# Kernel tuning notes

Hardware: AMD Instinct MI355X
Metric: run time of the kernel (lower is better)

Reference implementation:

```python
import jax, jax.numpy as jnp
import numpy as np

B, Q, K, D = 16, 2048, 2048, 512


def setup_inputs() -> dict:
    key = jax.random.key(0)
    kq, kk, kv, kl = jax.random.split(key, 4)
    queries = jax.random.normal(kq, (B, Q, D), dtype=jnp.float32)
    keys = jax.random.normal(kk, (B, K, D), dtype=jnp.float32)
    values = jax.random.normal(kv, (B, K, D), dtype=jnp.float32)
    # lengths in [1, K] so no row is fully masked
    valid_lens = jax.random.randint(kl, (B,), 1, K + 1, dtype=jnp.int32)
    return {"queries": queries, "keys": keys, "values": values, "valid_lens": valid_lens}


def reference(queries, keys, values, valid_lens):
    # scores: [B, Q, K]
    scale = 1.0 / jnp.sqrt(jnp.asarray(queries.shape[-1], queries.dtype))
    scores = jnp.einsum('bqd,bkd->bqk', queries, keys) * scale
    # 1D valid_lens: per-batch key-length mask (positions >= len are masked)
    key_pos = jnp.arange(scores.shape[-1])  # [K]
    mask = key_pos[None, None, :] >= valid_lens[:, None, None]  # [B, 1->Q, K]
    scores = jnp.where(mask, -jnp.inf, scores)
    weights = jax.nn.softmax(scores, axis=-1)  # [B, Q, K]
    # dropout is identity in eval mode (deterministic reference)
    context = jnp.einsum('bqk,bkd->bqd', weights, values)  # [B, Q, D]
    return context, weights
```

## Files before the change

kernel.cpp:

```cpp
#include <hip/hip_runtime.h>
#include <stdint.h>

typedef __bf16 bf16_t;
typedef bf16_t bf16x8 __attribute__((ext_vector_type(8)));
typedef bf16_t bf16x4_t __attribute__((ext_vector_type(4)));
typedef float f32x4 __attribute__((ext_vector_type(4)));

#define NB 16
#define NQ 2048
#define NK 2048
#define ND 512
#define SCALE 0.04419417382415922f

typedef __attribute__((address_space(3))) uint32_t lds_u32;
typedef __attribute__((address_space(1))) const uint32_t glb_u32;

__device__ __forceinline__ float4 ld4(const float* p) { return *(const float4*)p; }

__device__ __forceinline__ f32x4 mfma16(bf16x8 a, bf16x8 b, f32x4 c) {
  return __builtin_amdgcn_mfma_f32_16x16x32_bf16(a, b, c, 0, 0, 0);
}

__global__ __launch_bounds__(256) void prep_kernel(const float* __restrict__ Qf,
                                                   const float* __restrict__ Kf,
                                                   const float* __restrict__ Vf,
                                                   bf16_t* __restrict__ Qb,
                                                   bf16_t* __restrict__ Kb,
                                                   bf16_t* __restrict__ VT,
                                                   const int* __restrict__ lens) {
  int x = blockIdx.x;
  int b = blockIdx.y;
  int z = blockIdx.z;
  int t = threadIdx.x;

  if (z == 2) {
    int kb = x >> 2, dq = (x & 3) * 128;
    if (kb * 32 >= lens[b]) return;
    const float* vsrc = Vf + ((size_t)b * NK + kb * 32) * ND;
    bf16_t* dst = VT + ((size_t)(b * 64 + kb)) * (512 * 32);
    __shared__ alignas(16) bf16_t Ls[32][128];
#pragma unroll
    for (int i = 0; i < 4; ++i) {
      int p = i * 256 + t;
      int k = p >> 5, c4 = p & 31;
      float4 v = ld4(vsrc + (size_t)k * ND + dq + c4 * 4);
      union { bf16_t h[4]; uint2 u; } pk;
      pk.h[0] = (bf16_t)v.x; pk.h[1] = (bf16_t)v.y;
      pk.h[2] = (bf16_t)v.z; pk.h[3] = (bf16_t)v.w;
      *(uint2*)(&Ls[k][c4 * 4]) = pk.u;
    }
    __syncthreads();
    int d = dq + (t >> 1);
    int h = t & 1;
    int sr = d >> 1;
#pragma unroll
    for (int gg = 0; gg < 2; ++gg) {
      int g = h * 2 + gg;
      bf16x8 v;
#pragma unroll
      for (int j = 0; j < 8; ++j) v[j] = Ls[g * 8 + j][d - dq];
      int slot = (((d & 1) << 2) | g) ^ (sr & 7);
      *(bf16x8*)(dst + ((size_t)sr * 8 + slot) * 8) = v;
    }
    return;
  }

  const float* src = z ? Kf : Qf;
  bf16_t* dst = z ? Kb : Qb;
  int rt = x >> 4, kt = x & 15;
  const float* s = src + ((size_t)b * 2048 + (size_t)rt * 128) * 512 + kt * 32;
  bf16_t* dtile = dst + (((size_t)b * 16 + rt) * 16 + kt) * 4096;
#pragma unroll
  for (int i = 0; i < 2; ++i) {
    int d = i * 256 + t;
    int r = d >> 2, slot = d & 3;
    int c = slot ^ ((r >> 1) & 3);
    const float* p = s + (size_t)r * 512 + c * 8;
    float4 v0 = ld4(p), v1 = ld4(p + 4);
    bf16x8 o;
    o[0] = (bf16_t)v0.x; o[1] = (bf16_t)v0.y; o[2] = (bf16_t)v0.z; o[3] = (bf16_t)v0.w;
    o[4] = (bf16_t)v1.x; o[5] = (bf16_t)v1.y; o[6] = (bf16_t)v1.z; o[7] = (bf16_t)v1.w;
    *(bf16x8*)(dtile + (size_t)d * 8) = o;
  }
}

__global__ __launch_bounds__(512, 4) void qk_kernel(const bf16_t* __restrict__ Qb,
                                                    const bf16_t* __restrict__ Kb,
                                                    float* __restrict__ P,
                                                    float* __restrict__ psum,
                                                    const int* __restrict__ lens) {
  int bid = blockIdx.x;
  int swz = (bid & 7) * 256 + (bid >> 3);
  int b = swz >> 7;
  int qt = (swz >> 4) & 7;
  int nt = swz & 15;

  int len = lens[b];
  int q0 = qt * 256;
  int col0 = nt * 128;
  if (col0 >= len) return;

  __shared__ alignas(16) bf16_t As[2][8192];
  __shared__ alignas(16) bf16_t Bs[2][4096];
  __shared__ float rsm[256];

  int t = threadIdx.x;
  int lane = t & 63;
  int wid = t >> 6;
  int wm = wid >> 1, wn = wid & 1;
  int l15 = lane & 15, l4 = lane >> 4;

  float* prow = P + ((size_t)b * NQ + q0) * NK;
  const bf16_t* qbase = Qb + ((size_t)b * 256) * 4096;
  const bf16_t* ktile = Kb + (((size_t)b * 16 + nt) * 16) * 4096;

  f32x4 acc[4][4];
  f32x4 zz = {0.f, 0.f, 0.f, 0.f};
#pragma unroll
  for (int mi = 0; mi < 4; ++mi)
#pragma unroll
    for (int ni = 0; ni < 4; ++ni) acc[mi][ni] = zz;

  auto stage = [&](int kt2, int buf) {
#pragma unroll
    for (int u = 0; u < 2; ++u) {
      const bf16_t* qa = qbase + ((size_t)((qt * 2 + u) * 16 + kt2)) * 4096 + t * 8;
      __builtin_amdgcn_global_load_lds((glb_u32*)qa,
                                       (lds_u32*)(&As[buf][u * 4096 + wid * 512]), 16, 0, 0);
    }
    const bf16_t* ka = ktile + (size_t)kt2 * 4096 + t * 8;
    __builtin_amdgcn_global_load_lds((glb_u32*)ka,
                                     (lds_u32*)(&Bs[buf][wid * 512]), 16, 0, 0);
  };

  auto compute = [&](int buf) {
    bf16x8 af[4], bv[4];
#pragma unroll
    for (int mi = 0; mi < 4; ++mi) {
      int row = wm * 64 + mi * 16 + l15;
      int u = row >> 7, r7 = row & 127;
      int ch = r7 * 4 + (l4 ^ ((r7 >> 1) & 3));
      af[mi] = *(const bf16x8*)(&As[buf][u * 4096 + ch * 8]);
    }
#pragma unroll
    for (int ni = 0; ni < 4; ++ni) {
      int row = wn * 64 + ni * 16 + l15;
      int ch = row * 4 + (l4 ^ ((row >> 1) & 3));
      bv[ni] = *(const bf16x8*)(&Bs[buf][ch * 8]);
    }
#pragma unroll
    for (int mi = 0; mi < 4; ++mi)
#pragma unroll
      for (int ni = 0; ni < 4; ++ni)
        acc[mi][ni] = mfma16(af[mi], bv[ni], acc[mi][ni]);
  };

  stage(0, 0);
  __syncthreads();
#pragma unroll 1
  for (int kt2 = 0; kt2 < 16; ++kt2) {
    if (kt2 + 1 < 16) stage(kt2 + 1, (kt2 + 1) & 1);
    compute(kt2 & 1);
    __syncthreads();
  }

  float rsum[4][4];
#pragma unroll
  for (int mi = 0; mi < 4; ++mi)
#pragma unroll
    for (int r = 0; r < 4; ++r) rsum[mi][r] = 0.f;

#pragma unroll
  for (int mi = 0; mi < 4; ++mi) {
#pragma unroll
    for (int ni = 0; ni < 4; ++ni) {
      int col = col0 + wn * 64 + ni * 16 + l15;
      bool valid = col < len;
#pragma unroll
      for (int r = 0; r < 4; ++r) {
        float e = valid ? __expf(acc[mi][ni][r] * SCALE) : 0.f;
        bf16_t eb = (bf16_t)e;
        rsum[mi][r] += (float)eb;
        bf16_t* purow =
            (bf16_t*)(prow + (size_t)(wm * 64 + mi * 16 + l4 * 4 + r) * NK) + 2048;
        purow[col] = eb;
      }
    }
  }

#pragma unroll
  for (int off = 1; off < 16; off <<= 1)
#pragma unroll
    for (int mi = 0; mi < 4; ++mi)
#pragma unroll
      for (int r = 0; r < 4; ++r)
        rsum[mi][r] += __shfl_xor(rsum[mi][r], off, 64);

  if (wn == 0 && l15 == 0) {
#pragma unroll
    for (int mi = 0; mi < 4; ++mi)
#pragma unroll
      for (int r = 0; r < 4; ++r)
        rsm[wm * 64 + mi * 16 + l4 * 4 + r] = rsum[mi][r];
  }
  __syncthreads();
  if (wn == 1 && l15 == 0) {
#pragma unroll
    for (int mi = 0; mi < 4; ++mi)
#pragma unroll
      for (int r = 0; r < 4; ++r) {
        int row = wm * 64 + mi * 16 + l4 * 4 + r;
        psum[((size_t)b * 16 + nt) * NQ + q0 + row] = rsum[mi][r] + rsm[row];
      }
  }
}

__global__ __launch_bounds__(512, 4) void pv_kernel(float* __restrict__ P,
                                                    const bf16_t* __restrict__ VT,
                                                    float* __restrict__ ctx,
                                                    const float* __restrict__ psum,
                                                    const int* __restrict__ lens) {
  int bid = blockIdx.x;
  int b = bid & 15, qt = bid >> 4;
  int q0 = qt * 64;
  int len = lens[b];
  int nsteps = (len + 31) >> 5;
  int nvalid = (len + 127) >> 7;

  __shared__ alignas(16) bf16_t Ps[2][64 * 32];
  __shared__ float rcp[64];

  int t = threadIdx.x;
  if (t < 64) {
    float s = 0.f;
    for (int i = 0; i < nvalid; ++i) s += psum[((size_t)b * 16 + i) * NQ + q0 + t];
    rcp[t] = 1.0f / s;
  }
  __syncthreads();

  float* prow = P + ((size_t)b * NQ + q0) * NK;
  const bf16_t* vtb = VT + ((size_t)b * 64) * (512 * 32);

  int lane = t & 63, wid = t >> 6;
  int l15 = lane & 15, l4 = lane >> 4;

  f32x4 acc[4][4];
  f32x4 zz = {0.f, 0.f, 0.f, 0.f};
#pragma unroll
  for (int mi = 0; mi < 4; ++mi)
#pragma unroll
    for (int ni = 0; ni < 4; ++ni) acc[mi][ni] = zz;

  int srow = t >> 3, sc4 = t & 7;
  float rr = rcp[srow];
  const bf16_t* purow = (const bf16_t*)(prow + (size_t)srow * NK) + 2048;

  int vchunk[4];
#pragma unroll
  for (int ni = 0; ni < 4; ++ni) {
    int d = wid * 64 + ni * 16 + l15;
    vchunk[ni] = ((d >> 1) * 8 + ((((d & 1) << 2) | l4) ^ ((d >> 1) & 7))) * 8;
  }

  bf16x4_t pld;

  auto stage_load = [&](int ks) {
    pld = *(const bf16x4_t*)(purow + ks * 32 + sc4 * 4);
  };
  auto stage_finish = [&](int ks, int buf) {
    float4 w;
    w.x = (float)pld[0] * rr; w.y = (float)pld[1] * rr;
    w.z = (float)pld[2] * rr; w.w = (float)pld[3] * rr;
    *(float4*)(prow + (size_t)srow * NK + ks * 32 + sc4 * 4) = w;
    int sr = srow >> 1;
    int slot = (((srow & 1) << 2) | (sc4 >> 1)) ^ (sr & 7);
    union { bf16_t h[4]; uint2 u; } pk;
    pk.h[0] = (bf16_t)w.x; pk.h[1] = (bf16_t)w.y;
    pk.h[2] = (bf16_t)w.z; pk.h[3] = (bf16_t)w.w;
    *(uint2*)(&Ps[buf][((size_t)sr * 8 + slot) * 8 + (sc4 & 1) * 4]) = pk.u;
  };
  auto compute = [&](int ks, int cur) {
    const bf16_t* vsrc = vtb + (size_t)ks * (512 * 32);
    bf16x8 bv[4];
#pragma unroll
    for (int ni = 0; ni < 4; ++ni)
      bv[ni] = *(const bf16x8*)(vsrc + vchunk[ni]);
    bf16x8 af[4];
#pragma unroll
    for (int mi = 0; mi < 4; ++mi) {
      int row = mi * 16 + l15;
      af[mi] = *(const bf16x8*)(&Ps[cur][((row >> 1) * 8 + ((((row & 1) << 2) | l4) ^ ((row >> 1) & 7))) * 8]);
    }
#pragma unroll
    for (int mi = 0; mi < 4; ++mi)
#pragma unroll
      for (int ni = 0; ni < 4; ++ni)
        acc[mi][ni] = mfma16(af[mi], bv[ni], acc[mi][ni]);
  };

  stage_load(0);
  stage_finish(0, 0);
  __syncthreads();
#pragma unroll 1
  for (int ks = 0; ks < nsteps; ++ks) {
    int cur = ks & 1;
    if (ks + 1 < nsteps) stage_load(ks + 1);
    compute(ks, cur);
    if (ks + 1 < nsteps) stage_finish(ks + 1, cur ^ 1);
    __syncthreads();
  }

  {
    float4 z = make_float4(0.f, 0.f, 0.f, 0.f);
    for (int c = nsteps * 32 + sc4 * 4; c < NK; c += 32)
      *(float4*)(prow + (size_t)srow * NK + c) = z;
  }

  float* crow = ctx + ((size_t)b * NQ + q0) * ND + wid * 64;
#pragma unroll
  for (int mi = 0; mi < 4; ++mi)
#pragma unroll
    for (int ni = 0; ni < 4; ++ni)
#pragma unroll
      for (int r = 0; r < 4; ++r)
        crow[(size_t)(mi * 16 + l4 * 4 + r) * ND + ni * 16 + l15] = acc[mi][ni][r];
}

extern "C" void kernel_launch(void* const* d_in, const int* in_sizes, int n_in,
                              void* d_out, int out_size, void* d_ws, size_t ws_size,
                              hipStream_t stream) {
  const float* Q = (const float*)d_in[0];
  const float* K = (const float*)d_in[1];
  const float* V = (const float*)d_in[2];
  const int* lens = (const int*)d_in[3];

  float* ctx = (float*)d_out;
  float* P = ctx + (size_t)NB * NQ * ND;

  float* psum = (float*)d_ws;
  char* base = (char*)d_ws + (size_t)NB * 16 * NQ * sizeof(float);
  bf16_t* Qb = (bf16_t*)base;
  bf16_t* Kb = (bf16_t*)(base + (size_t)NB * NQ * ND * 2);
  bf16_t* VT = (bf16_t*)(base + (size_t)2 * NB * NQ * ND * 2);

  prep_kernel<<<dim3(256, 16, 3), 256, 0, stream>>>(Q, K, V, Qb, Kb, VT, lens);
  qk_kernel<<<dim3(2048), 512, 0, stream>>>(Qb, Kb, P, psum, lens);
  pv_kernel<<<dim3(512), 512, 0, stream>>>(P, VT, ctx, psum, lens);
}
```

Baseline: 271.1 us.

## Keep Q block resident in LDS and sweep all key tiles per QK block

The QK kernel now converts its 128-row fp32 Q block to bf16 directly into LDS once, then loops over all valid 256-column key tiles. It writes exp values per tile and accumulates row sums across tiles, so psum becomes one value per row instead of per-tile partials. This removes the Q conversion pass from the prep kernel and the repeated Q loads from global memory. In exchange, only 256 large blocks run at one block per CU (128KB LDS), and blocks whose batch has a long valid length do more work, which risks poor occupancy and load imbalance.

```diff
diff --git a/kernel.cpp b/kernel.cpp
--- a/kernel.cpp
+++ b/kernel.cpp
@@ -21,10 +21,8 @@
   return __builtin_amdgcn_mfma_f32_16x16x32_bf16(a, b, c, 0, 0, 0);
 }
 
-__global__ __launch_bounds__(256) void prep_kernel(const float* __restrict__ Qf,
-                                                   const float* __restrict__ Kf,
+__global__ __launch_bounds__(256) void prep_kernel(const float* __restrict__ Kf,
                                                    const float* __restrict__ Vf,
-                                                   bf16_t* __restrict__ Qb,
                                                    bf16_t* __restrict__ Kb,
                                                    bf16_t* __restrict__ VT,
                                                    const int* __restrict__ lens) {
@@ -33,7 +31,7 @@
   int z = blockIdx.z;
   int t = threadIdx.x;
 
-  if (z == 2) {
+  if (z == 1) {
     int kb = x >> 2, dq = (x & 3) * 128;
     if (kb * 32 >= lens[b]) return;
     const float* vsrc = Vf + ((size_t)b * NK + kb * 32) * ND;
@@ -65,11 +63,9 @@
     return;
   }
 
-  const float* src = z ? Kf : Qf;
-  bf16_t* dst = z ? Kb : Qb;
   int rt = x >> 4, kt = x & 15;
-  const float* s = src + ((size_t)b * 2048 + (size_t)rt * 128) * 512 + kt * 32;
-  bf16_t* dtile = dst + (((size_t)b * 16 + rt) * 16 + kt) * 4096;
+  const float* s = Kf + ((size_t)b * 2048 + (size_t)rt * 128) * 512 + kt * 32;
+  bf16_t* dtile = Kb + (((size_t)b * 16 + rt) * 16 + kt) * 4096;
 #pragma unroll
   for (int i = 0; i < 2; ++i) {
     int d = i * 256 + t;
@@ -84,35 +80,45 @@
   }
 }
 
-__global__ __launch_bounds__(512, 4) void qk_kernel(const bf16_t* __restrict__ Qb,
+__global__ __launch_bounds__(512, 1) void qk_kernel(const float* __restrict__ Qf,
                                                     const bf16_t* __restrict__ Kb,
                                                     float* __restrict__ P,
                                                     float* __restrict__ psum,
                                                     const int* __restrict__ lens) {
   int bid = blockIdx.x;
-  int swz = (bid & 7) * 256 + (bid >> 3);
-  int b = swz >> 7;
-  int qt = (swz >> 4) & 7;
-  int nt = swz & 15;
-
+  int b = bid & 15, qt = bid >> 4;
   int len = lens[b];
-  int q0 = qt * 256;
-  int col0 = nt * 128;
-  if (col0 >= len) return;
-
-  __shared__ alignas(16) bf16_t As[2][8192];
-  __shared__ alignas(16) bf16_t Bs[2][4096];
-  __shared__ float rsm[256];
+  int q0 = qt * 128;
+  int nvp = (len + 255) >> 8;
+  int nsteps = nvp * 16;
+
+  __shared__ alignas(16) bf16_t As[128 * 512];
+  __shared__ alignas(16) bf16_t Bs[2][256 * 32];
 
   int t = threadIdx.x;
   int lane = t & 63;
   int wid = t >> 6;
-  int wm = wid >> 1, wn = wid & 1;
+  int wm = wid >> 2, wn = wid & 3;
   int l15 = lane & 15, l4 = lane >> 4;
 
   float* prow = P + ((size_t)b * NQ + q0) * NK;
-  const bf16_t* qbase = Qb + ((size_t)b * 256) * 4096;
-  const bf16_t* ktile = Kb + (((size_t)b * 16 + nt) * 16) * 4096;
+  const bf16_t* kbase = Kb + ((size_t)b * 256) * 4096;
+
+  {
+    const float* qsrc = Qf + ((size_t)b * NQ + q0) * ND;
+#pragma unroll
+    for (int i = 0; i < 16; ++i) {
+      int g = i * 512 + t;
+      int row = g >> 6, ch = g & 63;
+      const float* p = qsrc + (size_t)row * ND + ch * 8;
+      float4 v0 = ld4(p), v1 = ld4(p + 4);
+      bf16x8 o;
+      o[0] = (bf16_t)v0.x; o[1] = (bf16_t)v0.y; o[2] = (bf16_t)v0.z; o[3] = (bf16_t)v0.w;
+      o[4] = (bf16_t)v1.x; o[5] = (bf16_t)v1.y; o[6] = (bf16_t)v1.z; o[7] = (bf16_t)v1.w;
+      int slot = (ch & 56) | ((ch & 7) ^ (row & 7));
+      *(bf16x8*)(&As[row * 512 + slot * 8]) = o;
+    }
+  }
 
   f32x4 acc[4][4];
   f32x4 zz = {0.f, 0.f, 0.f, 0.f};
@@ -121,32 +127,37 @@
 #pragma unroll
     for (int ni = 0; ni < 4; ++ni) acc[mi][ni] = zz;
 
-  auto stage = [&](int kt2, int buf) {
+  float rsum[4][4];
+#pragma unroll
+  for (int mi = 0; mi < 4; ++mi)
+#pragma unroll
+    for (int r = 0; r < 4; ++r) rsum[mi][r] = 0.f;
+
+  auto stage = [&](int s, int buf) {
+    int ntp = s >> 4, kt = s & 15;
 #pragma unroll
     for (int u = 0; u < 2; ++u) {
-      const bf16_t* qa = qbase + ((size_t)((qt * 2 + u) * 16 + kt2)) * 4096 + t * 8;
-      __builtin_amdgcn_global_load_lds((glb_u32*)qa,
-                                       (lds_u32*)(&As[buf][u * 4096 + wid * 512]), 16, 0, 0);
-    }
-    const bf16_t* ka = ktile + (size_t)kt2 * 4096 + t * 8;
-    __builtin_amdgcn_global_load_lds((glb_u32*)ka,
-                                     (lds_u32*)(&Bs[buf][wid * 512]), 16, 0, 0);
-  };
-
-  auto compute = [&](int buf) {
+      const bf16_t* ka = kbase + ((size_t)((ntp * 2 + u) * 16 + kt)) * 4096 + t * 8;
+      __builtin_amdgcn_global_load_lds((glb_u32*)ka,
+                                       (lds_u32*)(&Bs[buf][u * 4096 + wid * 512]), 16, 0, 0);
+    }
+  };
+
+  auto compute = [&](int kt, int buf) {
     bf16x8 af[4], bv[4];
 #pragma unroll
     for (int mi = 0; mi < 4; ++mi) {
       int row = wm * 64 + mi * 16 + l15;
-      int u = row >> 7, r7 = row & 127;
+      int ch = kt * 4 + l4;
+      int slot = (ch & 56) | ((ch & 7) ^ (row & 7));
+      af[mi] = *(const bf16x8*)(&As[row * 512 + slot * 8]);
+    }
+#pragma unroll
+    for (int ni = 0; ni < 4; ++ni) {
+      int c = wn * 64 + ni * 16 + l15;
+      int u = c >> 7, r7 = c & 127;
       int ch = r7 * 4 + (l4 ^ ((r7 >> 1) & 3));
-      af[mi] = *(const bf16x8*)(&As[buf][u * 4096 + ch * 8]);
-    }
-#pragma unroll
-    for (int ni = 0; ni < 4; ++ni) {
-      int row = wn * 64 + ni * 16 + l15;
-      int ch = row * 4 + (l4 ^ ((row >> 1) & 3));
-      bv[ni] = *(const bf16x8*)(&Bs[buf][ch * 8]);
+      bv[ni] = *(const bf16x8*)(&Bs[buf][u * 4096 + ch * 8]);
     }
 #pragma unroll
     for (int mi = 0; mi < 4; ++mi)
@@ -157,35 +168,33 @@
 
   stage(0, 0);
   __syncthreads();
+
 #pragma unroll 1
-  for (int kt2 = 0; kt2 < 16; ++kt2) {
-    if (kt2 + 1 < 16) stage(kt2 + 1, (kt2 + 1) & 1);
-    compute(kt2 & 1);
+  for (int s = 0; s < nsteps; ++s) {
+    if (s + 1 < nsteps) stage(s + 1, (s + 1) & 1);
+    compute(s & 15, s & 1);
+    if ((s & 15) == 15) {
+      int col0 = (s >> 4) * 256;
+#pragma unroll
+      for (int mi = 0; mi < 4; ++mi) {
+#pragma unroll
+        for (int ni = 0; ni < 4; ++ni) {
+          int col = col0 + wn * 64 + ni * 16 + l15;
+          bool valid = col < len;
+#pragma unroll
+          for (int r = 0; r < 4; ++r) {
+            float e = valid ? __expf(acc[mi][ni][r] * SCALE) : 0.f;
+            bf16_t eb = (bf16_t)e;
+            rsum[mi][r] += (float)eb;
+            bf16_t* purow =
+                (bf16_t*)(prow + (size_t)(wm * 64 + mi * 16 + l4 * 4 + r) * NK) + 2048;
+            purow[col] = eb;
+          }
+          acc[mi][ni] = zz;
+        }
+      }
+    }
     __syncthreads();
-  }
-
-  float rsum[4][4];
-#pragma unroll
-  for (int mi = 0; mi < 4; ++mi)
-#pragma unroll
-    for (int r = 0; r < 4; ++r) rsum[mi][r] = 0.f;
-
-#pragma unroll
-  for (int mi = 0; mi < 4; ++mi) {
-#pragma unroll
-    for (int ni = 0; ni < 4; ++ni) {
-      int col = col0 + wn * 64 + ni * 16 + l15;
-      bool valid = col < len;
-#pragma unroll
-      for (int r = 0; r < 4; ++r) {
-        float e = valid ? __expf(acc[mi][ni][r] * SCALE) : 0.f;
-        bf16_t eb = (bf16_t)e;
-        rsum[mi][r] += (float)eb;
-        bf16_t* purow =
-            (bf16_t*)(prow + (size_t)(wm * 64 + mi * 16 + l4 * 4 + r) * NK) + 2048;
-        purow[col] = eb;
-      }
-    }
   }
 
 #pragma unroll
@@ -196,23 +205,17 @@
       for (int r = 0; r < 4; ++r)
         rsum[mi][r] += __shfl_xor(rsum[mi][r], off, 64);
 
-  if (wn == 0 && l15 == 0) {
+  float* rsm = (float*)&Bs[0][0];
+  if (l15 == 0) {
 #pragma unroll
     for (int mi = 0; mi < 4; ++mi)
 #pragma unroll
       for (int r = 0; r < 4; ++r)
-        rsm[wm * 64 + mi * 16 + l4 * 4 + r] = rsum[mi][r];
+        rsm[wn * 128 + wm * 64 + mi * 16 + l4 * 4 + r] = rsum[mi][r];
   }
   __syncthreads();
-  if (wn == 1 && l15 == 0) {
-#pragma unroll
-    for (int mi = 0; mi < 4; ++mi)
-#pragma unroll
-      for (int r = 0; r < 4; ++r) {
-        int row = wm * 64 + mi * 16 + l4 * 4 + r;
-        psum[((size_t)b * 16 + nt) * NQ + q0 + row] = rsum[mi][r] + rsm[row];
-      }
-  }
+  if (t < 128)
+    psum[(size_t)b * NQ + q0 + t] = rsm[t] + rsm[128 + t] + rsm[256 + t] + rsm[384 + t];
 }
 
 __global__ __launch_bounds__(512, 4) void pv_kernel(float* __restrict__ P,
@@ -225,17 +228,12 @@
   int q0 = qt * 64;
   int len = lens[b];
   int nsteps = (len + 31) >> 5;
-  int nvalid = (len + 127) >> 7;
 
   __shared__ alignas(16) bf16_t Ps[2][64 * 32];
   __shared__ float rcp[64];
 
   int t = threadIdx.x;
-  if (t < 64) {
-    float s = 0.f;
-    for (int i = 0; i < nvalid; ++i) s += psum[((size_t)b * 16 + i) * NQ + q0 + t];
-    rcp[t] = 1.0f / s;
-  }
+  if (t < 64) rcp[t] = 1.0f / psum[(size_t)b * NQ + q0 + t];
   __syncthreads();
 
   float* prow = P + ((size_t)b * NQ + q0) * NK;
@@ -338,12 +336,11 @@
   float* P = ctx + (size_t)NB * NQ * ND;
 
   float* psum = (float*)d_ws;
-  char* base = (char*)d_ws + (size_t)NB * 16 * NQ * sizeof(float);
-  bf16_t* Qb = (bf16_t*)base;
-  bf16_t* Kb = (bf16_t*)(base + (size_t)NB * NQ * ND * 2);
-  bf16_t* VT = (bf16_t*)(base + (size_t)2 * NB * NQ * ND * 2);
-
-  prep_kernel<<<dim3(256, 16, 3), 256, 0, stream>>>(Q, K, V, Qb, Kb, VT, lens);
-  qk_kernel<<<dim3(2048), 512, 0, stream>>>(Qb, Kb, P, psum, lens);
+  char* base = (char*)d_ws + (size_t)NB * NQ * sizeof(float);
+  bf16_t* Kb = (bf16_t*)base;
+  bf16_t* VT = (bf16_t*)(base + (size_t)NB * NQ * ND * 2);
+
+  prep_kernel<<<dim3(256, 16, 2), 256, 0, stream>>>(K, V, Kb, VT, lens);
+  qk_kernel<<<dim3(256), 512, 0, stream>>>(Q, Kb, P, psum, lens);
   pv_kernel<<<dim3(512), 512, 0, stream>>>(P, VT, ctx, psum, lens);
 }
```

Result: slower. 306.5 us (+13.1%).

## Make PV kernel persistent with atomic work queue and 32-row query tiles

Applied to the files above, without the earlier changes.

The PV kernel becomes persistent: 512 blocks repeatedly take work items from a global atomic counter, and each item covers a 32-query tile rather than a 64-query tile, giving 1024 items. The aim is to balance the uneven per-batch work caused by variable valid lengths, since long-length batches no longer pin whole blocks while others sit idle. In exchange only half the threads stage P in each item, each V fragment is reused across fewer rows, and every launch adds a memset plus an atomic and extra barriers per item.

```diff
diff --git a/kernel.cpp b/kernel.cpp
--- a/kernel.cpp
+++ b/kernel.cpp
@@ -11,6 +11,7 @@
 #define NK 2048
 #define ND 512
 #define SCALE 0.04419417382415922f
+#define NITEMS 1024
 
 typedef __attribute__((address_space(3))) uint32_t lds_u32;
 typedef __attribute__((address_space(1))) const uint32_t glb_u32;
@@ -219,41 +220,16 @@
                                                     const bf16_t* __restrict__ VT,
                                                     float* __restrict__ ctx,
                                                     const float* __restrict__ psum,
-                                                    const int* __restrict__ lens) {
-  int bid = blockIdx.x;
-  int b = bid & 15, qt = bid >> 4;
-  int q0 = qt * 64;
-  int len = lens[b];
-  int nsteps = (len + 31) >> 5;
-  int nvalid = (len + 127) >> 7;
-
-  __shared__ alignas(16) bf16_t Ps[2][64 * 32];
-  __shared__ float rcp[64];
+                                                    const int* __restrict__ lens,
+                                                    int* __restrict__ counter) {
+  __shared__ alignas(16) bf16_t Ps[2][32 * 32];
+  __shared__ float rcp[32];
+  __shared__ int itm;
 
   int t = threadIdx.x;
-  if (t < 64) {
-    float s = 0.f;
-    for (int i = 0; i < nvalid; ++i) s += psum[((size_t)b * 16 + i) * NQ + q0 + t];
-    rcp[t] = 1.0f / s;
-  }
-  __syncthreads();
-
-  float* prow = P + ((size_t)b * NQ + q0) * NK;
-  const bf16_t* vtb = VT + ((size_t)b * 64) * (512 * 32);
-
   int lane = t & 63, wid = t >> 6;
   int l15 = lane & 15, l4 = lane >> 4;
-
-  f32x4 acc[4][4];
-  f32x4 zz = {0.f, 0.f, 0.f, 0.f};
-#pragma unroll
-  for (int mi = 0; mi < 4; ++mi)
-#pragma unroll
-    for (int ni = 0; ni < 4; ++ni) acc[mi][ni] = zz;
-
   int srow = t >> 3, sc4 = t & 7;
-  float rr = rcp[srow];
-  const bf16_t* purow = (const bf16_t*)(prow + (size_t)srow * NK) + 2048;
 
   int vchunk[4];
 #pragma unroll
@@ -262,68 +238,105 @@
     vchunk[ni] = ((d >> 1) * 8 + ((((d & 1) << 2) | l4) ^ ((d >> 1) & 7))) * 8;
   }
 
-  bf16x4_t pld;
-
-  auto stage_load = [&](int ks) {
-    pld = *(const bf16x4_t*)(purow + ks * 32 + sc4 * 4);
-  };
-  auto stage_finish = [&](int ks, int buf) {
-    float4 w;
-    w.x = (float)pld[0] * rr; w.y = (float)pld[1] * rr;
-    w.z = (float)pld[2] * rr; w.w = (float)pld[3] * rr;
-    *(float4*)(prow + (size_t)srow * NK + ks * 32 + sc4 * 4) = w;
-    int sr = srow >> 1;
-    int slot = (((srow & 1) << 2) | (sc4 >> 1)) ^ (sr & 7);
-    union { bf16_t h[4]; uint2 u; } pk;
-    pk.h[0] = (bf16_t)w.x; pk.h[1] = (bf16_t)w.y;
-    pk.h[2] = (bf16_t)w.z; pk.h[3] = (bf16_t)w.w;
-    *(uint2*)(&Ps[buf][((size_t)sr * 8 + slot) * 8 + (sc4 & 1) * 4]) = pk.u;
-  };
-  auto compute = [&](int ks, int cur) {
-    const bf16_t* vsrc = vtb + (size_t)ks * (512 * 32);
-    bf16x8 bv[4];
-#pragma unroll
-    for (int ni = 0; ni < 4; ++ni)
-      bv[ni] = *(const bf16x8*)(vsrc + vchunk[ni]);
-    bf16x8 af[4];
-#pragma unroll
-    for (int mi = 0; mi < 4; ++mi) {
-      int row = mi * 16 + l15;
-      af[mi] = *(const bf16x8*)(&Ps[cur][((row >> 1) * 8 + ((((row & 1) << 2) | l4) ^ ((row >> 1) & 7))) * 8]);
-    }
-#pragma unroll
-    for (int mi = 0; mi < 4; ++mi)
+  for (;;) {
+    if (t == 0) itm = atomicAdd(counter, 1);
+    __syncthreads();
+    int item = itm;
+    if (item >= NITEMS) break;
+    int b = item >> 6;
+    int qt = item & 63;
+    int q0 = qt * 32;
+    int len = lens[b];
+    int nsteps = (len + 31) >> 5;
+    int nvalid = (len + 127) >> 7;
+
+    if (t < 32) {
+      float s = 0.f;
+      for (int i = 0; i < nvalid; ++i) s += psum[((size_t)b * 16 + i) * NQ + q0 + t];
+      rcp[t] = 1.0f / s;
+    }
+    __syncthreads();
+
+    float* prow = P + ((size_t)b * NQ + q0) * NK;
+    const bf16_t* vtb = VT + ((size_t)b * 64) * (512 * 32);
+    float rr = (t < 256) ? rcp[srow] : 0.f;
+    const bf16_t* purow = (const bf16_t*)(prow + (size_t)srow * NK) + 2048;
+
+    f32x4 acc[2][4];
+    f32x4 zz = {0.f, 0.f, 0.f, 0.f};
+#pragma unroll
+    for (int mi = 0; mi < 2; ++mi)
+#pragma unroll
+      for (int ni = 0; ni < 4; ++ni) acc[mi][ni] = zz;
+
+    bf16x4_t pld;
+    auto stage_load = [&](int ks) {
+      if (t < 256) pld = *(const bf16x4_t*)(purow + ks * 32 + sc4 * 4);
+    };
+    auto stage_finish = [&](int ks, int buf) {
+      if (t < 256) {
+        float4 w;
+        w.x = (float)pld[0] * rr; w.y = (float)pld[1] * rr;
+        w.z = (float)pld[2] * rr; w.w = (float)pld[3] * rr;
+        *(float4*)(prow + (size_t)srow * NK + ks * 32 + sc4 * 4) = w;
+        int sr = srow >> 1;
+        int slot = (((srow & 1) << 2) | (sc4 >> 1)) ^ (sr & 7);
+        union { bf16_t h[4]; uint2 u; } pk;
+        pk.h[0] = (bf16_t)w.x; pk.h[1] = (bf16_t)w.y;
+        pk.h[2] = (bf16_t)w.z; pk.h[3] = (bf16_t)w.w;
+        *(uint2*)(&Ps[buf][((size_t)sr * 8 + slot) * 8 + (sc4 & 1) * 4]) = pk.u;
+      }
+    };
+    auto compute = [&](int ks, int cur) {
+      const bf16_t* vsrc = vtb + (size_t)ks * (512 * 32);
+      bf16x8 bv[4];
 #pragma unroll
       for (int ni = 0; ni < 4; ++ni)
-        acc[mi][ni] = mfma16(af[mi], bv[ni], acc[mi][ni]);
-  };
-
-  stage_load(0);
-  stage_finish(0, 0);
-  __syncthreads();
+        bv[ni] = *(const bf16x8*)(vsrc + vchunk[ni]);
+      bf16x8 af[2];
+#pragma unroll
+      for (int mi = 0; mi < 2; ++mi) {
+        int row = mi * 16 + l15;
+        af[mi] = *(const bf16x8*)(&Ps[cur][((row >> 1) * 8 + ((((row & 1) << 2) | l4) ^ ((row >> 1) & 7))) * 8]);
+      }
+#pragma unroll
+      for (int mi = 0; mi < 2; ++mi)
+#pragma unroll
+        for (int ni = 0; ni < 4; ++ni)
+          acc[mi][ni] = mfma16(af[mi], bv[ni], acc[mi][ni]);
+    };
+
+    stage_load(0);
+    stage_finish(0, 0);
+    __syncthreads();
 #pragma unroll 1
-  for (int ks = 0; ks < nsteps; ++ks) {
-    int cur = ks & 1;
-    if (ks + 1 < nsteps) stage_load(ks + 1);
-    compute(ks, cur);
-    if (ks + 1 < nsteps) stage_finish(ks + 1, cur ^ 1);
-    __syncthreads();
-  }
-
-  {
-    float4 z = make_float4(0.f, 0.f, 0.f, 0.f);
-    for (int c = nsteps * 32 + sc4 * 4; c < NK; c += 32)
-      *(float4*)(prow + (size_t)srow * NK + c) = z;
-  }
-
-  float* crow = ctx + ((size_t)b * NQ + q0) * ND + wid * 64;
-#pragma unroll
-  for (int mi = 0; mi < 4; ++mi)
-#pragma unroll
-    for (int ni = 0; ni < 4; ++ni)
-#pragma unroll
-      for (int r = 0; r < 4; ++r)
-        crow[(size_t)(mi * 16 + l4 * 4 + r) * ND + ni * 16 + l15] = acc[mi][ni][r];
+    for (int ks = 0; ks < nsteps; ++ks) {
+      int cur = ks & 1;
+      if (ks + 1 < nsteps) stage_load(ks + 1);
+      compute(ks, cur);
+      if (ks == 62 && nsteps == 64) __syncthreads();
+      if (ks + 1 < nsteps) stage_finish(ks + 1, cur ^ 1);
+      __syncthreads();
+    }
+
+    {
+      float4 z = make_float4(0.f, 0.f, 0.f, 0.f);
+      int zr = t >> 4, zc = t & 15;
+      for (int c = nsteps * 32 + zc * 4; c < NK; c += 64)
+        *(float4*)(prow + (size_t)zr * NK + c) = z;
+    }
+
+    float* crow = ctx + ((size_t)b * NQ + q0) * ND + wid * 64;
+#pragma unroll
+    for (int mi = 0; mi < 2; ++mi)
+#pragma unroll
+      for (int ni = 0; ni < 4; ++ni)
+#pragma unroll
+        for (int r = 0; r < 4; ++r)
+          crow[(size_t)(mi * 16 + l4 * 4 + r) * ND + ni * 16 + l15] = acc[mi][ni][r];
+
+    __syncthreads();
+  }
 }
 
 extern "C" void kernel_launch(void* const* d_in, const int* in_sizes, int n_in,
@@ -342,8 +355,10 @@
   bf16_t* Qb = (bf16_t*)base;
   bf16_t* Kb = (bf16_t*)(base + (size_t)NB * NQ * ND * 2);
   bf16_t* VT = (bf16_t*)(base + (size_t)2 * NB * NQ * ND * 2);
+  int* counter = (int*)(base + (size_t)3 * NB * NQ * ND * 2);
 
   prep_kernel<<<dim3(256, 16, 3), 256, 0, stream>>>(Q, K, V, Qb, Kb, VT, lens);
   qk_kernel<<<dim3(2048), 512, 0, stream>>>(Qb, Kb, P, psum, lens);
-  pv_kernel<<<dim3(512), 512, 0, stream>>>(P, VT, ctx, psum, lens);
-}
+  hipMemsetAsync(counter, 0, sizeof(int), stream);
+  pv_kernel<<<dim3(512), 512, 0, stream>>>(P, VT, ctx, psum, lens, counter);
+}
```

New measurement: 309.2 us. 14.0% more time.

## Split weight normalization out of PV kernel and defer context scaling

Applied to the files above, without the earlier changes.

The PV kernel now only stages the unnormalized bf16 probabilities (stored in the upper half of each P row) into LDS and runs the MFMA, then scales the context output by the per-row reciprocal sum at the end. A new wnorm kernel afterwards reads the bf16 data, normalizes it, writes the fp32 weights and zeroes masked columns across the full row. The aim is to take the global fp32 weight stores out of the MFMA loop and use a simple streaming kernel for them. This adds a kernel launch and a second read of the bf16 data, and relies on running wnorm after ctx because both use the same buffer.

```diff
diff --git a/kernel.cpp b/kernel.cpp
--- a/kernel.cpp
+++ b/kernel.cpp
@@ -215,11 +215,11 @@
   }
 }
 
-__global__ __launch_bounds__(512, 4) void pv_kernel(float* __restrict__ P,
-                                                    const bf16_t* __restrict__ VT,
-                                                    float* __restrict__ ctx,
-                                                    const float* __restrict__ psum,
-                                                    const int* __restrict__ lens) {
+__global__ __launch_bounds__(512, 4) void ctx_kernel(const float* __restrict__ P,
+                                                     const bf16_t* __restrict__ VT,
+                                                     float* __restrict__ ctx,
+                                                     const float* __restrict__ psum,
+                                                     const int* __restrict__ lens) {
   int bid = blockIdx.x;
   int b = bid & 15, qt = bid >> 4;
   int q0 = qt * 64;
@@ -238,7 +238,7 @@
   }
   __syncthreads();
 
-  float* prow = P + ((size_t)b * NQ + q0) * NK;
+  const float* prow = P + ((size_t)b * NQ + q0) * NK;
   const bf16_t* vtb = VT + ((size_t)b * 64) * (512 * 32);
 
   int lane = t & 63, wid = t >> 6;
@@ -252,7 +252,6 @@
     for (int ni = 0; ni < 4; ++ni) acc[mi][ni] = zz;
 
   int srow = t >> 3, sc4 = t & 7;
-  float rr = rcp[srow];
   const bf16_t* purow = (const bf16_t*)(prow + (size_t)srow * NK) + 2048;
 
   int vchunk[4];
@@ -267,16 +266,11 @@
   auto stage_load = [&](int ks) {
     pld = *(const bf16x4_t*)(purow + ks * 32 + sc4 * 4);
   };
-  auto stage_finish = [&](int ks, int buf) {
-    float4 w;
-    w.x = (float)pld[0] * rr; w.y = (float)pld[1] * rr;
-    w.z = (float)pld[2] * rr; w.w = (float)pld[3] * rr;
-    *(float4*)(prow + (size_t)srow * NK + ks * 32 + sc4 * 4) = w;
+  auto stage_finish = [&](int buf) {
     int sr = srow >> 1;
     int slot = (((srow & 1) << 2) | (sc4 >> 1)) ^ (sr & 7);
-    union { bf16_t h[4]; uint2 u; } pk;
-    pk.h[0] = (bf16_t)w.x; pk.h[1] = (bf16_t)w.y;
-    pk.h[2] = (bf16_t)w.z; pk.h[3] = (bf16_t)w.w;
+    union { bf16x4_t v; uint2 u; } pk;
+    pk.v = pld;
     *(uint2*)(&Ps[buf][((size_t)sr * 8 + slot) * 8 + (sc4 & 1) * 4]) = pk.u;
   };
   auto compute = [&](int ks, int cur) {
@@ -299,23 +293,17 @@
   };
 
   stage_load(0);
-  stage_finish(0, 0);
+  stage_finish(0);
   __syncthreads();
 #pragma unroll 1
   for (int ks = 0; ks < nsteps; ++ks) {
     int cur = ks & 1;
     if (ks + 1 < nsteps) stage_load(ks + 1);
     compute(ks, cur);
-    if (ks + 1 < nsteps) stage_finish(ks + 1, cur ^ 1);
+    if (ks + 1 < nsteps) stage_finish(cur ^ 1);
     __syncthreads();
   }
 
-  {
-    float4 z = make_float4(0.f, 0.f, 0.f, 0.f);
-    for (int c = nsteps * 32 + sc4 * 4; c < NK; c += 32)
-      *(float4*)(prow + (size_t)srow * NK + c) = z;
-  }
-
   float* crow = ctx + ((size_t)b * NQ + q0) * ND + wid * 64;
 #pragma unroll
   for (int mi = 0; mi < 4; ++mi)
@@ -323,7 +311,51 @@
     for (int ni = 0; ni < 4; ++ni)
 #pragma unroll
       for (int r = 0; r < 4; ++r)
-        crow[(size_t)(mi * 16 + l4 * 4 + r) * ND + ni * 16 + l15] = acc[mi][ni][r];
+        crow[(size_t)(mi * 16 + l4 * 4 + r) * ND + ni * 16 + l15] =
+            acc[mi][ni][r] * rcp[mi * 16 + l4 * 4 + r];
+}
+
+__global__ __launch_bounds__(256) void wnorm_kernel(float* __restrict__ P,
+                                                    const float* __restrict__ psum,
+                                                    const int* __restrict__ lens) {
+  int bid = blockIdx.x;
+  int b = bid & 15;
+  int q0 = (bid >> 4) * 8;
+  int len = lens[b];
+  int nvalid = (len + 127) >> 7;
+
+  __shared__ float rcp[8];
+  int t = threadIdx.x;
+  if (t < 8) {
+    float s = 0.f;
+    for (int i = 0; i < nvalid; ++i) s += psum[((size_t)b * 16 + i) * NQ + q0 + t];
+    rcp[t] = 1.0f / s;
+  }
+
+  int row = t >> 5, ck = t & 31;
+  float* prow = P + ((size_t)b * NQ + q0 + row) * NK;
+  const bf16_t* pu = (const bf16_t*)prow + 2048 + ck * 64;
+
+  bf16x8 v[8];
+#pragma unroll
+  for (int i = 0; i < 8; ++i) v[i] = *(const bf16x8*)(pu + i * 8);
+  __syncthreads();
+
+  float rr = rcp[row];
+  int colbase = ck * 64;
+#pragma unroll
+  for (int i = 0; i < 8; ++i) {
+    f32x4 w0, w1;
+#pragma unroll
+    for (int j = 0; j < 4; ++j) {
+      int c0 = colbase + i * 8 + j;
+      int c1 = c0 + 4;
+      w0[j] = (c0 < len) ? (float)v[i][j] * rr : 0.f;
+      w1[j] = (c1 < len) ? (float)v[i][j + 4] * rr : 0.f;
+    }
+    *(f32x4*)(prow + colbase + i * 8) = w0;
+    *(f32x4*)(prow + colbase + i * 8 + 4) = w1;
+  }
 }
 
 extern "C" void kernel_launch(void* const* d_in, const int* in_sizes, int n_in,
@@ -345,5 +377,6 @@
 
   prep_kernel<<<dim3(256, 16, 3), 256, 0, stream>>>(Q, K, V, Qb, Kb, VT, lens);
   qk_kernel<<<dim3(2048), 512, 0, stream>>>(Qb, Kb, P, psum, lens);
-  pv_kernel<<<dim3(512), 512, 0, stream>>>(P, VT, ctx, psum, lens);
-}
+  ctx_kernel<<<dim3(512), 512, 0, stream>>>(P, VT, ctx, psum, lens);
+  wnorm_kernel<<<dim3(4096), 256, 0, stream>>>(P, psum, lens);
+}
```

New measurement: 324.8 us. +19.8%, slower.
